# Kernel tuning notes

Measured on AMD Instinct MI355X. Metric: run time of the kernel, lower is better.

The kernel has to match this reference:

```python
import jax, jax.numpy as jnp
import numpy as np

H = 8            # n_heads
CLIP = 10.0      # tanh_clipping
CAPACITY = 1.0   # AgentVRP.VEHICLE_CAPACITY


def setup_inputs() -> dict:
    key = jax.random.key(0)
    ks = jax.random.split(key, 12)
    B, N, D = 256, 1000, 128
    s = 1.0 / np.sqrt(D)  # keep pre-tanh logits in a sane range
    return {
        "embeddings": jax.random.normal(ks[0], (B, N, D), jnp.float32),
        "mean_graph_emb": jax.random.normal(ks[1], (B, D), jnp.float32),
        "used_capacity": jax.random.uniform(ks[2], (B, 1), jnp.float32),
        "prev_node": jax.random.randint(ks[3], (B, 1), 0, N),
        "mask": jax.random.randint(ks[4], (B, 1, N), 0, 2).astype(bool),
        "wq_context": jax.random.normal(ks[5], (D, D), jnp.float32) * s,
        "wq_step_context": jax.random.normal(ks[6], (D + 1, D), jnp.float32) * s,
        "wk": jax.random.normal(ks[7], (D, D), jnp.float32) * s,
        "wk_tanh": jax.random.normal(ks[8], (D, D), jnp.float32) * s,
        "wv": jax.random.normal(ks[9], (D, D), jnp.float32) * s,
        "w_out": jax.random.normal(ks[10], (D, D), jnp.float32) * s,
    }


def reference(embeddings, mean_graph_emb, used_capacity, prev_node, mask,
              wq_context, wq_step_context, wk, wk_tanh, wv, w_out):
    B, N, D = embeddings.shape
    hd = D // H
    neg_inf = jnp.float32(-np.inf)

    # --- get_projections ---
    K = (embeddings @ wk).reshape(B, N, H, hd).transpose(0, 2, 1, 3)       # bhnd
    V = (embeddings @ wv).reshape(B, N, H, hd).transpose(0, 2, 1, 3)       # bhnd
    K_tanh = embeddings @ wk_tanh                                          # bnD
    Q_context = (mean_graph_emb @ wq_context)[:, None, :]                  # b1D

    # --- get_step_context ---
    cur = jnp.take_along_axis(embeddings, prev_node[:, :, None].astype(jnp.int32), axis=1)  # b1D
    step_ctx = jnp.concatenate([cur, CAPACITY - used_capacity[:, :, None]], axis=-1)        # b1(D+1)
    Q = Q_context + step_ctx @ wq_step_context                             # b1D
    Qh = Q.reshape(B, 1, H, hd).transpose(0, 2, 1, 3)                      # bh1d

    # --- decoder_mha (seq_len_q = 1) ---
    compat = jnp.einsum('bhqd,bhnd->bhqn', Qh, K) / jnp.sqrt(jnp.float32(hd))
    compat = jnp.where(mask[:, None, :, :], neg_inf, compat)
    attn = jax.nn.softmax(compat, axis=-1)
    out = jnp.einsum('bhqn,bhnd->bhqd', attn, V)
    mha = out.transpose(0, 2, 1, 3).reshape(B, 1, D) @ w_out               # b1D

    # --- get_log_p (single head, tanh-clipped) ---
    logits = jnp.einsum('bqD,bnD->bqn', mha, K_tanh) / jnp.sqrt(jnp.float32(D))
    logits = jnp.tanh(logits) * CLIP
    logits = jnp.where(mask, neg_inf, logits)
    log_p = jax.nn.log_softmax(logits, axis=-1)                            # b1n
    return log_p
```

## Files before the change

kernel.cpp:

```cpp
#include <hip/hip_runtime.h>
#include <hip/hip_bf16.h>
#include <math.h>

constexpr int kB = 256;
constexpr int kN = 1000;
constexpr int kD = 128;
constexpr int kH = 8;

#define MASK_FILL (-1.0e30f)

__device__ __forceinline__ bool is_masked(const void* m, int flag, int idx) {
  if (flag == 1) return ((const unsigned char*)m)[idx] != 0;
  if (flag == 0) return ((const int*)m)[idx] != 0;
  return ((const float*)m)[idx] != 0.0f;
}

__global__ __launch_bounds__(128) void q_kernel(
    const float* __restrict__ emb, const float* __restrict__ mge,
    const float* __restrict__ ucap, const int* __restrict__ prev,
    const float* __restrict__ wq_ctx, const float* __restrict__ wq_step,
    const float* __restrict__ wk, float* __restrict__ qt,
    const unsigned char* __restrict__ mb, int* __restrict__ flag) {
  const int b = blockIdx.x, t = threadIdx.x;
  __shared__ float cur[kD];
  __shared__ float Qs[kD];
  __shared__ int nonbin, off123;
  if (b == 0 && t == 0) { nonbin = 0; off123 = 0; }
  const float* crow = emb + ((size_t)b * kN + prev[b]) * kD;
  cur[t] = crow[t];
  __syncthreads();
  if (b == 0) {
    int l_nonbin = 0, l_off = 0;
    for (int i = t; i < 4096; i += 128) {
      unsigned char v = mb[i];
      if (v > 1) l_nonbin = 1;
      if (v != 0 && (i & 3) != 0) l_off = 1;
    }
    if (l_nonbin) atomicOr(&nonbin, 1);
    if (l_off) atomicOr(&off123, 1);
  }
  float acc = 0.f;
  const float* mger = mge + (size_t)b * kD;
  #pragma unroll 4
  for (int e = 0; e < kD; ++e) {
    acc += mger[e] * wq_ctx[e * kD + t];
    acc += cur[e] * wq_step[e * kD + t];
  }
  acc += (1.0f - ucap[b]) * wq_step[kD * kD + t];
  Qs[t] = acc;
  __syncthreads();
  if (b == 0 && t == 0) *flag = nonbin ? 2 : (off123 ? 1 : 0);
  float a8[8] = {};
  const float* wkrow = wk + (size_t)t * kD;
  #pragma unroll
  for (int h = 0; h < 8; ++h) {
    #pragma unroll
    for (int j = 0; j < 16; ++j)
      a8[h] += wkrow[h * 16 + j] * Qs[h * 16 + j];
  }
  #pragma unroll
  for (int h = 0; h < 8; ++h)
    qt[((size_t)b * 8 + h) * kD + t] = a8[h] * 0.25f;
}

__global__ __launch_bounds__(256, 2) void attn_part_kernel(
    const float* __restrict__ emb, const float* __restrict__ qt_g,
    const void* __restrict__ mask, const int* __restrict__ flagp,
    float* __restrict__ pw, float* __restrict__ pl,
    int nsplit, int rows_per) {
  const int s = blockIdx.x, b = blockIdx.y, t = threadIdx.x;
  __shared__ __align__(16) float tile[32][132];
  __shared__ __align__(16) float qts[8][160];
  __shared__ __align__(16) float wl[32][8];
  __shared__ float lred[4][8];
  __shared__ unsigned char mloc[512];
  const int flag = *flagp;
  const int rowstart = s * rows_per;
  const int nrows = min(rows_per, kN - rowstart);
  const int row = t >> 3, seg = t & 7;
  for (int idx = t; idx < 1024; idx += 256) {
    const int h = idx >> 7, d = idx & 127;
    qts[h][(d >> 4) * 20 + (d & 15)] = qt_g[((size_t)b << 10) + idx];
  }
  for (int i = t; i < nrows; i += 256)
    mloc[i] = is_masked(mask, flag, b * kN + rowstart + i) ? 1 : 0;
  const float* embb = emb + (size_t)b * kN * kD;
  const int d4 = t & 31, hh = (t >> 5) & 1, rgrp = t >> 6;
  float4 a0 = {}, a1 = {}, a2 = {}, a3 = {};
  float l0 = 0.f, l1 = 0.f, l2 = 0.f, l3 = 0.f;
  const int ntiles = (nrows + 31) >> 5;
  float4 rc0, rc1, rc2, rc3;
  {
    const int lr = row < nrows ? row : 0;
    const float* src = embb + (size_t)(rowstart + lr) * kD + seg * 16;
    rc0 = *reinterpret_cast<const float4*>(src);
    rc1 = *reinterpret_cast<const float4*>(src + 4);
    rc2 = *reinterpret_cast<const float4*>(src + 8);
    rc3 = *reinterpret_cast<const float4*>(src + 12);
  }
  __syncthreads();
  for (int ti = 0; ti < ntiles; ++ti) {
    const int lrow = ti * 32 + row;
    {
      float* dst = &tile[row][seg * 16];
      *reinterpret_cast<float4*>(dst)      = rc0;
      *reinterpret_cast<float4*>(dst + 4)  = rc1;
      *reinterpret_cast<float4*>(dst + 8)  = rc2;
      *reinterpret_cast<float4*>(dst + 12) = rc3;
    }
    float4 rn0, rn1, rn2, rn3;
    const bool more = ti + 1 < ntiles;
    if (more) {
      int lr = (ti + 1) * 32 + row; if (lr >= nrows) lr = 0;
      const float* src = embb + (size_t)(rowstart + lr) * kD + seg * 16;
      rn0 = *reinterpret_cast<const float4*>(src);
      rn1 = *reinterpret_cast<const float4*>(src + 4);
      rn2 = *reinterpret_cast<const float4*>(src + 8);
      rn3 = *reinterpret_cast<const float4*>(src + 12);
    }
    {
      float p0 = 0, p1 = 0, p2 = 0, p3 = 0, p4 = 0, p5 = 0, p6 = 0, p7 = 0;
      #pragma unroll
      for (int j4 = 0; j4 < 4; ++j4) {
        const float4 e = j4 == 0 ? rc0 : j4 == 1 ? rc1 : j4 == 2 ? rc2 : rc3;
        const int qoff = seg * 20 + j4 * 4;
        #define SCORE_H(ph, h) { \
          const float4 q = *reinterpret_cast<const float4*>(&qts[h][qoff]); \
          ph += e.x * q.x + e.y * q.y + e.z * q.z + e.w * q.w; }
        SCORE_H(p0, 0) SCORE_H(p1, 1) SCORE_H(p2, 2) SCORE_H(p3, 3)
        SCORE_H(p4, 4) SCORE_H(p5, 5) SCORE_H(p6, 6) SCORE_H(p7, 7)
        #undef SCORE_H
      }
      #define RED(ph) ph += __shfl_xor(ph, 1, 64); ph += __shfl_xor(ph, 2, 64); \
                      ph += __shfl_xor(ph, 4, 64);
      RED(p0) RED(p1) RED(p2) RED(p3) RED(p4) RED(p5) RED(p6) RED(p7)
      #undef RED
      const float myp = seg == 0 ? p0 : seg == 1 ? p1 : seg == 2 ? p2 :
                        seg == 3 ? p3 : seg == 4 ? p4 : seg == 5 ? p5 :
                        seg == 6 ? p6 : p7;
      const bool ok = (lrow < nrows) && (mloc[lrow] == 0);
      wl[row][seg] = ok ? __expf(myp) : 0.f;
    }
    __syncthreads();
    #pragma unroll
    for (int rr = 0; rr < 8; ++rr) {
      const int r = rgrp * 8 + rr;
      const float4 e = *reinterpret_cast<const float4*>(&tile[r][d4 * 4]);
      const float4 w = *reinterpret_cast<const float4*>(&wl[r][hh * 4]);
      a0.x += w.x * e.x; a0.y += w.x * e.y; a0.z += w.x * e.z; a0.w += w.x * e.w;
      a1.x += w.y * e.x; a1.y += w.y * e.y; a1.z += w.y * e.z; a1.w += w.y * e.w;
      a2.x += w.z * e.x; a2.y += w.z * e.y; a2.z += w.z * e.z; a2.w += w.z * e.w;
      a3.x += w.w * e.x; a3.y += w.w * e.y; a3.z += w.w * e.z; a3.w += w.w * e.w;
      l0 += w.x; l1 += w.y; l2 += w.z; l3 += w.w;
    }
    __syncthreads();
    if (more) { rc0 = rn0; rc1 = rn1; rc2 = rn2; rc3 = rn3; }
  }
  float* tf = &tile[0][0];
  *reinterpret_cast<float4*>(&tf[t * 16])      = a0;
  *reinterpret_cast<float4*>(&tf[t * 16 + 4])  = a1;
  *reinterpret_cast<float4*>(&tf[t * 16 + 8])  = a2;
  *reinterpret_cast<float4*>(&tf[t * 16 + 12]) = a3;
  if (d4 == 0) {
    lred[rgrp][hh * 4]     = l0; lred[rgrp][hh * 4 + 1] = l1;
    lred[rgrp][hh * 4 + 2] = l2; lred[rgrp][hh * 4 + 3] = l3;
  }
  __syncthreads();
  for (int o = t; o < 1024; o += 256) {
    const int h = o >> 7, d = o & 127;
    const int c = d & 3, dd4 = d >> 2, hh2 = h >> 2, hi = h & 3;
    float v = 0.f;
    #pragma unroll
    for (int g = 0; g < 4; ++g)
      v += tf[(((g * 2 + hh2) * 32) + dd4) * 16 + hi * 4 + c];
    pw[(size_t)(b * nsplit + s) * 1024 + o] = v;
  }
  if (t < 8)
    pl[(size_t)(b * nsplit + s) * kH + t] =
        lred[0][t] + lred[1][t] + lred[2][t] + lred[3][t];
}

__global__ __launch_bounds__(1024) void logits_all_kernel(
    const float* __restrict__ emb, const void* __restrict__ mask,
    const float* __restrict__ pw, const float* __restrict__ pl,
    const float* __restrict__ wv_w, const float* __restrict__ w_out,
    const float* __restrict__ wk_tanh, float* __restrict__ out, int nsplit) {
  const int b = blockIdx.x, t = threadIdx.x;
  __shared__ float wsuml[8][132];
  __shared__ float outflat[128];
  __shared__ float mhal[128];
  __shared__ float mtl[128];
  __shared__ float linv[8];
  __shared__ float tl[kN];
  __shared__ float sums[16];
  __shared__ int nonbin_s, off_s;
  if (t == 0) { nonbin_s = 0; off_s = 0; }
  if (t < 8) {
    float l = 0.f;
    for (int s2 = 0; s2 < nsplit; ++s2)
      l += pl[(size_t)(b * nsplit + s2) * kH + t];
    linv[t] = 1.0f / l;
  }
  __syncthreads();
  {
    const unsigned char* mb = (const unsigned char*)mask;
    int ln = 0, lo = 0;
    for (int i = t; i < 4096; i += 1024) {
      const unsigned char v = mb[i];
      if (v > 1) ln = 1;
      if (v != 0 && (i & 3) != 0) lo = 1;
    }
    if (ln) atomicOr(&nonbin_s, 1);
    if (lo) atomicOr(&off_s, 1);
  }
  {
    const int h = t >> 7, d = t & 127;
    float v = 0.f;
    for (int s2 = 0; s2 < nsplit; ++s2)
      v += pw[(size_t)(b * nsplit + s2) * 1024 + t];
    wsuml[h][d] = v * linv[h];
  }
  __syncthreads();
  const int flag = nonbin_s ? 2 : (off_s ? 1 : 0);
  const int j = t >> 3, sg = t & 7;
  {
    const int h = j >> 4;
    float pp = 0.f;
    #pragma unroll
    for (int jj = 0; jj < 16; ++jj) {
      const int d = sg * 16 + jj;
      pp += wsuml[h][d] * wv_w[(size_t)d * kD + j];
    }
    pp += __shfl_xor(pp, 1, 64);
    pp += __shfl_xor(pp, 2, 64);
    pp += __shfl_xor(pp, 4, 64);
    if (sg == 0) outflat[j] = pp;
  }
  __syncthreads();
  {
    float pp = 0.f;
    #pragma unroll
    for (int jj = 0; jj < 16; ++jj) {
      const int d = sg * 16 + jj;
      pp += outflat[d] * w_out[(size_t)d * kD + j];
    }
    pp += __shfl_xor(pp, 1, 64);
    pp += __shfl_xor(pp, 2, 64);
    pp += __shfl_xor(pp, 4, 64);
    if (sg == 0) mhal[j] = pp;
  }
  __syncthreads();
  {
    float pp = 0.f;
    const float* wr = wk_tanh + (size_t)j * kD + sg * 16;
    #pragma unroll
    for (int jj = 0; jj < 16; ++jj)
      pp += wr[jj] * mhal[sg * 16 + jj];
    pp += __shfl_xor(pp, 1, 64);
    pp += __shfl_xor(pp, 2, 64);
    pp += __shfl_xor(pp, 4, 64);
    if (sg == 0) mtl[j] = pp * 0.08838834764831845f;
  }
  __syncthreads();
  const int seg = t & 7, r8 = t >> 3;
  const float* mtb = &mtl[seg * 16];
  const float4 m0 = *reinterpret_cast<const float4*>(mtb);
  const float4 m1 = *reinterpret_cast<const float4*>(mtb + 4);
  const float4 m2 = *reinterpret_cast<const float4*>(mtb + 8);
  const float4 m3 = *reinterpret_cast<const float4*>(mtb + 12);
  float sumexp = 0.f;
  const float* embb = emb + (size_t)b * kN * kD;
  #pragma unroll
  for (int it = 0; it < 8; ++it) {
    const int n = it * 128 + r8;
    const bool valid = n < kN;
    const int nc = valid ? n : kN - 1;
    const float* row = embb + (size_t)nc * kD + seg * 16;
    const float4 e0 = *reinterpret_cast<const float4*>(row);
    const float4 e1 = *reinterpret_cast<const float4*>(row + 4);
    const float4 e2 = *reinterpret_cast<const float4*>(row + 8);
    const float4 e3 = *reinterpret_cast<const float4*>(row + 12);
    float p = e0.x * m0.x + e0.y * m0.y + e0.z * m0.z + e0.w * m0.w
            + e1.x * m1.x + e1.y * m1.y + e1.z * m1.z + e1.w * m1.w
            + e2.x * m2.x + e2.y * m2.y + e2.z * m2.z + e2.w * m2.w
            + e3.x * m3.x + e3.y * m3.y + e3.z * m3.z + e3.w * m3.w;
    p += __shfl_xor(p, 1, 64);
    p += __shfl_xor(p, 2, 64);
    p += __shfl_xor(p, 4, 64);
    if (valid && seg == 0) {
      if (is_masked(mask, flag, b * kN + n)) {
        tl[n] = MASK_FILL;
      } else {
        const float tv = tanhf(p) * 10.0f;
        tl[n] = tv;
        sumexp += __expf(tv);
      }
    }
  }
  #pragma unroll
  for (int off = 1; off < 64; off <<= 1)
    sumexp += __shfl_xor(sumexp, off, 64);
  if ((t & 63) == 0) sums[t >> 6] = sumexp;
  __syncthreads();
  if (t < kN) {
    float total = 0.f;
    #pragma unroll
    for (int i = 0; i < 16; ++i) total += sums[i];
    const float lse = logf(total);
    const float v = tl[t];
    out[(size_t)b * kN + t] = (v == MASK_FILL) ? MASK_FILL : v - lse;
  }
}

extern "C" void kernel_launch(void* const* d_in, const int* in_sizes, int n_in,
                              void* d_out, int out_size, void* d_ws, size_t ws_size,
                              hipStream_t stream) {
  const float* emb     = (const float*)d_in[0];
  const float* mge     = (const float*)d_in[1];
  const float* ucap    = (const float*)d_in[2];
  const int*   prev    = (const int*)d_in[3];
  const void*  mask    = d_in[4];
  const float* wq_ctx  = (const float*)d_in[5];
  const float* wq_step = (const float*)d_in[6];
  const float* wk      = (const float*)d_in[7];
  const float* wk_tanh = (const float*)d_in[8];
  const float* wv_w    = (const float*)d_in[9];
  const float* w_out   = (const float*)d_in[10];
  float* out = (float*)d_out;

  const size_t flag_off = 0;
  const size_t qt_off   = 256;
  const size_t qt_sz    = (size_t)kB * kH * kD * 4;
  const size_t pw_off   = qt_off + qt_sz;
  auto need = [&](int ns) {
    return pw_off + (size_t)kB * ns * (kH * kD + kH) * 4;
  };
  const int nsplit = (ws_size >= need(4)) ? 4 : 2;
  const int rows_per = (kN + nsplit - 1) / nsplit;
  const size_t pw_sz = (size_t)kB * nsplit * kH * kD * 4;

  int*   flag = (int*)((char*)d_ws + flag_off);
  float* qt   = (float*)((char*)d_ws + qt_off);
  float* pw   = (float*)((char*)d_ws + pw_off);
  float* pl   = (float*)((char*)d_ws + pw_off + pw_sz);

  hipLaunchKernelGGL(q_kernel, dim3(kB), dim3(128), 0, stream,
                     emb, mge, ucap, prev, wq_ctx, wq_step, wk, qt,
                     (const unsigned char*)mask, flag);
  hipLaunchKernelGGL(attn_part_kernel, dim3(nsplit, kB), dim3(256), 0, stream,
                     emb, qt, mask, flag, pw, pl, nsplit, rows_per);
  hipLaunchKernelGGL(logits_all_kernel, dim3(kB), dim3(1024), 0, stream,
                     emb, mask, pw, pl, wv_w, w_out, wk_tanh, out, nsplit);
}
```

Measured before the change: 95.55 us.

## Double-buffer attention tiles, halve tile rows, and split sequence eight ways

```diff
diff --git a/kernel.cpp b/kernel.cpp
--- a/kernel.cpp
+++ b/kernel.cpp
@@ -69,15 +69,15 @@
     float* __restrict__ pw, float* __restrict__ pl,
     int nsplit, int rows_per) {
   const int s = blockIdx.x, b = blockIdx.y, t = threadIdx.x;
-  __shared__ __align__(16) float tile[32][132];
+  __shared__ __align__(16) float tile[2][16][132];
   __shared__ __align__(16) float qts[8][160];
-  __shared__ __align__(16) float wl[32][8];
+  __shared__ __align__(16) float wl[2][16][8];
   __shared__ float lred[4][8];
-  __shared__ unsigned char mloc[512];
+  __shared__ unsigned char mloc[128];
   const int flag = *flagp;
   const int rowstart = s * rows_per;
   const int nrows = min(rows_per, kN - rowstart);
-  const int row = t >> 3, seg = t & 7;
+  const int row = t >> 4, sp = t & 15;
   for (int idx = t; idx < 1024; idx += 256) {
     const int h = idx >> 7, d = idx & 127;
     qts[h][(d >> 4) * 20 + (d & 15)] = qt_g[((size_t)b << 10) + idx];
@@ -88,42 +88,38 @@
   const int d4 = t & 31, hh = (t >> 5) & 1, rgrp = t >> 6;
   float4 a0 = {}, a1 = {}, a2 = {}, a3 = {};
   float l0 = 0.f, l1 = 0.f, l2 = 0.f, l3 = 0.f;
-  const int ntiles = (nrows + 31) >> 5;
-  float4 rc0, rc1, rc2, rc3;
+  const int ntiles = (nrows + 15) >> 4;
+  float4 rc0, rc1;
   {
     const int lr = row < nrows ? row : 0;
-    const float* src = embb + (size_t)(rowstart + lr) * kD + seg * 16;
+    const float* src = embb + (size_t)(rowstart + lr) * kD + sp * 8;
     rc0 = *reinterpret_cast<const float4*>(src);
     rc1 = *reinterpret_cast<const float4*>(src + 4);
-    rc2 = *reinterpret_cast<const float4*>(src + 8);
-    rc3 = *reinterpret_cast<const float4*>(src + 12);
   }
   __syncthreads();
   for (int ti = 0; ti < ntiles; ++ti) {
-    const int lrow = ti * 32 + row;
+    const int cur = ti & 1;
+    const int lrow = ti * 16 + row;
     {
-      float* dst = &tile[row][seg * 16];
-      *reinterpret_cast<float4*>(dst)      = rc0;
-      *reinterpret_cast<float4*>(dst + 4)  = rc1;
-      *reinterpret_cast<float4*>(dst + 8)  = rc2;
-      *reinterpret_cast<float4*>(dst + 12) = rc3;
-    }
-    float4 rn0, rn1, rn2, rn3;
+      float* dst = &tile[cur][row][sp * 8];
+      *reinterpret_cast<float4*>(dst)     = rc0;
+      *reinterpret_cast<float4*>(dst + 4) = rc1;
+    }
+    float4 rn0, rn1;
     const bool more = ti + 1 < ntiles;
     if (more) {
-      int lr = (ti + 1) * 32 + row; if (lr >= nrows) lr = 0;
-      const float* src = embb + (size_t)(rowstart + lr) * kD + seg * 16;
+      int lr = (ti + 1) * 16 + row; if (lr >= nrows) lr = 0;
+      const float* src = embb + (size_t)(rowstart + lr) * kD + sp * 8;
       rn0 = *reinterpret_cast<const float4*>(src);
       rn1 = *reinterpret_cast<const float4*>(src + 4);
-      rn2 = *reinterpret_cast<const float4*>(src + 8);
-      rn3 = *reinterpret_cast<const float4*>(src + 12);
     }
     {
       float p0 = 0, p1 = 0, p2 = 0, p3 = 0, p4 = 0, p5 = 0, p6 = 0, p7 = 0;
       #pragma unroll
-      for (int j4 = 0; j4 < 4; ++j4) {
-        const float4 e = j4 == 0 ? rc0 : j4 == 1 ? rc1 : j4 == 2 ? rc2 : rc3;
-        const int qoff = seg * 20 + j4 * 4;
+      for (int j4 = 0; j4 < 2; ++j4) {
+        const float4 e = j4 == 0 ? rc0 : rc1;
+        const int dbase = sp * 8 + j4 * 4;
+        const int qoff = (dbase >> 4) * 20 + (dbase & 15);
         #define SCORE_H(ph, h) { \
           const float4 q = *reinterpret_cast<const float4*>(&qts[h][qoff]); \
           ph += e.x * q.x + e.y * q.y + e.z * q.z + e.w * q.w; }
@@ -132,31 +128,33 @@
         #undef SCORE_H
       }
       #define RED(ph) ph += __shfl_xor(ph, 1, 64); ph += __shfl_xor(ph, 2, 64); \
-                      ph += __shfl_xor(ph, 4, 64);
+                      ph += __shfl_xor(ph, 4, 64); ph += __shfl_xor(ph, 8, 64);
       RED(p0) RED(p1) RED(p2) RED(p3) RED(p4) RED(p5) RED(p6) RED(p7)
       #undef RED
-      const float myp = seg == 0 ? p0 : seg == 1 ? p1 : seg == 2 ? p2 :
-                        seg == 3 ? p3 : seg == 4 ? p4 : seg == 5 ? p5 :
-                        seg == 6 ? p6 : p7;
-      const bool ok = (lrow < nrows) && (mloc[lrow] == 0);
-      wl[row][seg] = ok ? __expf(myp) : 0.f;
+      if (sp < 8) {
+        const float myp = sp == 0 ? p0 : sp == 1 ? p1 : sp == 2 ? p2 :
+                          sp == 3 ? p3 : sp == 4 ? p4 : sp == 5 ? p5 :
+                          sp == 6 ? p6 : p7;
+        const bool ok = (lrow < nrows) && (mloc[lrow] == 0);
+        wl[cur][row][sp] = ok ? __expf(myp) : 0.f;
+      }
     }
     __syncthreads();
     #pragma unroll
-    for (int rr = 0; rr < 8; ++rr) {
-      const int r = rgrp * 8 + rr;
-      const float4 e = *reinterpret_cast<const float4*>(&tile[r][d4 * 4]);
-      const float4 w = *reinterpret_cast<const float4*>(&wl[r][hh * 4]);
+    for (int rr = 0; rr < 4; ++rr) {
+      const int r = rgrp * 4 + rr;
+      const float4 e = *reinterpret_cast<const float4*>(&tile[cur][r][d4 * 4]);
+      const float4 w = *reinterpret_cast<const float4*>(&wl[cur][r][hh * 4]);
       a0.x += w.x * e.x; a0.y += w.x * e.y; a0.z += w.x * e.z; a0.w += w.x * e.w;
       a1.x += w.y * e.x; a1.y += w.y * e.y; a1.z += w.y * e.z; a1.w += w.y * e.w;
       a2.x += w.z * e.x; a2.y += w.z * e.y; a2.z += w.z * e.z; a2.w += w.z * e.w;
       a3.x += w.w * e.x; a3.y += w.w * e.y; a3.z += w.w * e.z; a3.w += w.w * e.w;
       l0 += w.x; l1 += w.y; l2 += w.z; l3 += w.w;
     }
-    __syncthreads();
-    if (more) { rc0 = rn0; rc1 = rn1; rc2 = rn2; rc3 = rn3; }
-  }
-  float* tf = &tile[0][0];
+    if (more) { rc0 = rn0; rc1 = rn1; }
+  }
+  __syncthreads();
+  float* tf = &tile[0][0][0];
   *reinterpret_cast<float4*>(&tf[t * 16])      = a0;
   *reinterpret_cast<float4*>(&tf[t * 16 + 4])  = a1;
   *reinterpret_cast<float4*>(&tf[t * 16 + 8])  = a2;
@@ -335,7 +333,9 @@
   auto need = [&](int ns) {
     return pw_off + (size_t)kB * ns * (kH * kD + kH) * 4;
   };
-  const int nsplit = (ws_size >= need(4)) ? 4 : 2;
+  int nsplit = 2;
+  if (ws_size >= need(8)) nsplit = 8;
+  else if (ws_size >= need(4)) nsplit = 4;
   const int rows_per = (kN + nsplit - 1) / nsplit;
   const size_t pw_sz = (size_t)kB * nsplit * kH * kD * 4;
 
```

Measured after the change: 108.4 us. 13.5% more time.
